# Performance work log

Hardware: AMD Instinct MI355X
Metric: run time of the kernel (lower is better)

## Reference

```python
import jax, jax.numpy as jnp
import numpy as np

EPS = 1e-8       # module eps
LN_EPS = 1e-5    # torch LayerNorm default
TEMP = 1.0       # relevance_temperature
STRENGTH = 1.0   # reweight_strength default (None -> 1.0)

Q, W, A = 64, 16, 64
D, C, H = 512, 512, 512


def _ln(x, g, b):
    m = x.mean(-1, keepdims=True)
    v = ((x - m) ** 2).mean(-1, keepdims=True)
    return (x - m) / jnp.sqrt(v + LN_EPS) * g + b


def _mlp(x, g, b, w1, b1, w2, b2):
    # LayerNorm -> Linear -> GELU(exact) -> Linear
    h = jax.nn.gelu(_ln(x, g, b) @ w1 + b1, approximate=False)
    return h @ w2 + b2


def setup_inputs() -> dict:
    key = jax.random.key(0)
    ks = iter(jax.random.split(key, 40))
    s = 0.02

    def lin(din, dout):
        return (jax.random.normal(next(ks), (din, dout), jnp.float32) * s,
                jnp.zeros((dout,), jnp.float32))

    inp = {
        "query_atoms": jax.random.normal(next(ks), (Q, A, D), jnp.float32),
        "query_masses": jax.random.uniform(next(ks), (Q, A), jnp.float32, 0.01, 1.0),
        "class_atoms": jax.random.normal(next(ks), (W, A, D), jnp.float32),
        "class_masses": jax.random.uniform(next(ks), (W, A), jnp.float32, 0.01, 1.0),
        "class_summary": jax.random.normal(next(ks), (W, C), jnp.float32),
        "episode_context": jax.random.normal(next(ks), (W, C), jnp.float32),
    }
    # query_proj
    inp["qg"], inp["qb"] = jnp.ones((D,), jnp.float32), jnp.zeros((D,), jnp.float32)
    inp["qw1"], inp["qb1"] = lin(D, H)
    inp["qw2"], inp["qb2"] = lin(H, H)
    # atom_proj
    inp["ag"], inp["ab"] = jnp.ones((D,), jnp.float32), jnp.zeros((D,), jnp.float32)
    inp["aw1"], inp["ab1"] = lin(D, H)
    inp["aw2"], inp["ab2"] = lin(H, H)
    # context_proj (input 2*C)
    inp["cg"], inp["cb"] = jnp.ones((2 * C,), jnp.float32), jnp.zeros((2 * C,), jnp.float32)
    inp["cw1"], inp["cb1"] = lin(2 * C, H)
    inp["cw2"], inp["cb2"] = lin(H, H)
    # relevance_head (input 4*H, output 1)
    inp["rg"], inp["rb"] = jnp.ones((4 * H,), jnp.float32), jnp.zeros((4 * H,), jnp.float32)
    inp["rw1"], inp["rb1"] = lin(4 * H, H)
    inp["rw2"], inp["rb2"] = lin(H, 1)
    return inp


def reference(query_atoms, query_masses, class_atoms, class_masses,
              class_summary, episode_context,
              qg, qb, qw1, qb1, qw2, qb2,
              ag, ab, aw1, ab1, aw2, ab2,
              cg, cb, cw1, cb1, cw2, cb2,
              rg, rb, rw1, rb1, rw2, rb2):
    # normalize query masses, pool query atoms -> [Q, D]
    qm = jnp.maximum(query_masses, 0.0)
    qm = qm / jnp.maximum(qm.sum(-1, keepdims=True), EPS)
    pooled = jnp.einsum('qa,qad->qd', qm, query_atoms)

    qh = _mlp(pooled, qg, qb, qw1, qb1, qw2, qb2)            # [Q, H]
    ah = _mlp(class_atoms, ag, ab, aw1, ab1, aw2, ab2)       # [W, A, H]
    ch = _mlp(jnp.concatenate([class_summary, episode_context], -1),
              cg, cb, cw1, cb1, cw2, cb2)                    # [W, H]

    nq, (way, na, h) = qh.shape[0], ah.shape
    a4 = jnp.broadcast_to(ah[None], (nq, way, na, h))
    q4 = jnp.broadcast_to(qh[:, None, None, :], (nq, way, na, h))
    c4 = jnp.broadcast_to(ch[None, :, None, :], (nq, way, na, h))
    fused = jnp.concatenate([a4, q4, a4 * q4, jnp.abs(a4 - q4) + c4], -1)  # [Q,W,A,4H]

    relevance = _mlp(fused, rg, rb, rw1, rb1, rw2, rb2)[..., 0]  # [Q, W, A]

    combined = jnp.log(jnp.maximum(class_masses, EPS))[None] + relevance / TEMP
    rew = jax.nn.softmax(combined, axis=-1)
    mixed = (1.0 - STRENGTH) * class_masses[None] + STRENGTH * rew
    mixed = mixed / jnp.maximum(mixed.sum(-1, keepdims=True), EPS)
    entropy = -(mixed * jnp.log(jnp.maximum(mixed, EPS))).sum(-1)  # [Q, W]
    return mixed, entropy
```

## Files before the change

kernel.cpp:

```cpp
#include <hip/hip_runtime.h>


#define DEV static __device__ __forceinline__

typedef __attribute__((ext_vector_type(8))) __bf16 bf16x8;
typedef __attribute__((ext_vector_type(4))) float f32x4;
typedef unsigned short ushort_t;

DEV ushort_t f2bf(float f) {
  unsigned u = __builtin_bit_cast(unsigned, f);
  u = (u + 0x7fffu + ((u >> 16) & 1u)) >> 16;
  return (ushort_t)u;
}

DEV float gelu_fast(float x) {
  const float y = x * 0.70710678118654752f;
  const float z = fabsf(y);
  const float t = __fdividef(1.0f, 1.0f + 0.3275911f * z);
  float p = 1.061405429f;
  p = p * t - 1.453152027f;
  p = p * t + 1.421413741f;
  p = p * t - 0.284496736f;
  p = p * t + 0.254829592f;
  const float e = 1.0f - p * t * __expf(-z * z);
  const float erfv = copysignf(e, y);
  return 0.5f * x * (1.0f + erfv);
}

DEV float gelu_sig(float x) {
  return x * __frcp_rn(1.0f + __expf(-1.702f * x));
}

#define OFF_XQB    0
#define OFF_XAB    16384
#define OFF_XCB    278528
#define OFF_HAB    286720
#define OFF_HQB    548864
#define OFF_HCB    565248
#define OFF_AHB    569344
#define OFF_QH     1093632
#define OFF_S1     1126400
#define OFF_B1     1126912
#define OFF_WT2    1127424
#define OFF_RW1LOT 1389568
#define OFF_RW1MIT 1520640
#define OFF_AW1T   1651712
#define OFF_QW1T   1782784
#define OFF_CW1T   1913856
#define OFF_AW2T   2176000
#define OFF_QW2T   2307072
#define OFF_CW2T   2438144
#define OFF_YA     OFF_AW1T
#define OFF_YQ     OFF_AW2T
#define OFF_CHH    OFF_XCB
#define OFF_AHHS   OFF_XAB
#define OFF_QHS    OFF_XQB


DEV void transpose_tile(const float* __restrict__ src, int koff, int kt, int ct,
                        ushort_t* __restrict__ dst, int ldk, float* sh, int tid) {
  float (*t)[65] = (float(*)[65])sh;
  for (int idx = tid; idx < 4096; idx += 512) {
    const int r = idx >> 6, c = idx & 63;
    t[r][c] = src[(koff + kt + r) * 512 + ct + c];
  }
  __syncthreads();
  for (int idx = tid; idx < 4096; idx += 512) {
    const int c = idx >> 6, r = idx & 63;
    dst[(ct + c) * ldk + kt + r] = f2bf(t[r][c]);
  }
}

__global__ __launch_bounds__(512) void pre0_kernel(
    const float* __restrict__ qa, const float* __restrict__ qm,
    const float* __restrict__ ca, const float* __restrict__ csum,
    const float* __restrict__ ectx,
    const float* __restrict__ qg, const float* __restrict__ qb,
    const float* __restrict__ ag, const float* __restrict__ ab,
    const float* __restrict__ cg, const float* __restrict__ cb,
    const float* __restrict__ rw1, const float* __restrict__ rg,
    const float* __restrict__ rb,
    const float* __restrict__ aw1, const float* __restrict__ qw1,
    const float* __restrict__ cw1, const float* __restrict__ aw2,
    const float* __restrict__ qw2, const float* __restrict__ cw2,
    float* __restrict__ ws) {
  __shared__ float sh[4160];
  const int b = blockIdx.x, tid = threadIdx.x, l = tid & 63, wv = tid >> 6;

  if (b < 128) {
    ushort_t* WT = (ushort_t*)(ws + OFF_WT2);
    float (*t)[65] = (float(*)[65])sh;
    const int kt = (b >> 3) << 6;
    const int ct = (b & 7) << 6;
    for (int idx = tid; idx < 4096; idx += 512) {
      const int r = idx >> 6, c = idx & 63;
      t[r][c] = rg[1024 + kt + r] * rw1[(1024 + kt + r) * 512 + ct + c];
    }
    __syncthreads();
    for (int idx = tid; idx < 4096; idx += 512) {
      const int c = idx >> 6, r = idx & 63;
      const int n = ct + c, k2 = kt + r;
      WT[((k2 >> 5) << 14) + (n << 5) + (k2 & 31)] = f2bf(t[r][c]);
    }
  } else if (b < 192) {
    const int bb = b - 128;
    transpose_tile(rw1, 0, (bb >> 3) << 6, (bb & 7) << 6,
                   (ushort_t*)(ws + OFF_RW1LOT), 512, sh, tid);
  } else if (b < 256) {
    const int bb = b - 192;
    transpose_tile(rw1, 512, (bb >> 3) << 6, (bb & 7) << 6,
                   (ushort_t*)(ws + OFF_RW1MIT), 512, sh, tid);
  } else if (b < 320) {
    const int bb = b - 256;
    transpose_tile(aw1, 0, (bb >> 3) << 6, (bb & 7) << 6,
                   (ushort_t*)(ws + OFF_AW1T), 512, sh, tid);
  } else if (b < 384) {
    const int bb = b - 320;
    transpose_tile(qw1, 0, (bb >> 3) << 6, (bb & 7) << 6,
                   (ushort_t*)(ws + OFF_QW1T), 512, sh, tid);
  } else if (b < 512) {
    const int bb = b - 384;
    transpose_tile(cw1, 0, (bb >> 3) << 6, (bb & 7) << 6,
                   (ushort_t*)(ws + OFF_CW1T), 1024, sh, tid);
  } else if (b < 576) {
    const int bb = b - 512;
    transpose_tile(aw2, 0, (bb >> 3) << 6, (bb & 7) << 6,
                   (ushort_t*)(ws + OFF_AW2T), 512, sh, tid);
  } else if (b < 640) {
    const int bb = b - 576;
    transpose_tile(qw2, 0, (bb >> 3) << 6, (bb & 7) << 6,
                   (ushort_t*)(ws + OFF_QW2T), 512, sh, tid);
  } else if (b < 704) {
    const int bb = b - 640;
    transpose_tile(cw2, 0, (bb >> 3) << 6, (bb & 7) << 6,
                   (ushort_t*)(ws + OFF_CW2T), 512, sh, tid);
  } else if (b < 720) {
    const int kc = (b - 704) << 7;
    float s0 = 0.f, s1 = 0.f, b0 = 0.f, b1v = 0.f;
    for (int k = kc; k < kc + 128; k += 2) {
      const float wa = rw1[(k << 9) + tid];
      const float wb = rw1[((k + 1) << 9) + tid];
      s0 += rg[k] * wa; b0 += rb[k] * wa;
      s1 += rg[k + 1] * wb; b1v += rb[k + 1] * wb;
    }
    atomicAdd(ws + OFF_S1 + tid, s0 + s1);
    atomicAdd(ws + OFF_B1 + tid, b0 + b1v);
  } else if (b < 784) {
    const int q = b - 720;
    if (wv == 0) {
      float m = fmaxf(qm[(q << 6) + l], 0.f);
      sh[l] = m;
      float s = m;
#pragma unroll
      for (int off = 1; off < 64; off <<= 1) s += __shfl_xor(s, off);
      if (l == 0) sh[64] = 1.0f / fmaxf(s, 1e-8f);
    }
    __syncthreads();
    const float sinv = sh[64];
    const float* qaq = qa + (q << 15) + tid;
    float v0 = 0.f, v1 = 0.f, v2 = 0.f, v3 = 0.f;
#pragma unroll 4
    for (int a = 0; a < 64; a += 4) {
      v0 += sh[a] * qaq[a << 9];
      v1 += sh[a + 1] * qaq[(a + 1) << 9];
      v2 += sh[a + 2] * qaq[(a + 2) << 9];
      v3 += sh[a + 3] * qaq[(a + 3) << 9];
    }
    const float v = (v0 + v1 + v2 + v3) * sinv;
    float s = v, ss = v * v;
#pragma unroll
    for (int off = 1; off < 64; off <<= 1) {
      s += __shfl_xor(s, off); ss += __shfl_xor(ss, off);
    }
    if (l == 0) { sh[128 + wv] = s; sh[136 + wv] = ss; }
    __syncthreads();
    float st = 0.f, sst = 0.f;
#pragma unroll
    for (int i = 0; i < 8; ++i) { st += sh[128 + i]; sst += sh[136 + i]; }
    const float mu = st * (1.0f / 512.0f);
    const float rstd = rsqrtf(sst * (1.0f / 512.0f) - mu * mu + 1e-5f);
    ((ushort_t*)(ws + OFF_XQB))[(q << 9) + tid] =
        f2bf((v - mu) * rstd * qg[tid] + qb[tid]);
  } else if (b < 912) {
    const int row = ((b - 784) << 3) + wv;
    const float* crow = ca + (row << 9);
    float x[8];
    float s = 0.f, ss = 0.f;
#pragma unroll
    for (int i = 0; i < 8; ++i) {
      x[i] = crow[l + (i << 6)];
      s += x[i]; ss += x[i] * x[i];
    }
#pragma unroll
    for (int off = 1; off < 64; off <<= 1) {
      s += __shfl_xor(s, off); ss += __shfl_xor(ss, off);
    }
    const float mu = s * (1.0f / 512.0f);
    const float rstd = rsqrtf(ss * (1.0f / 512.0f) - mu * mu + 1e-5f);
    ushort_t* xab = (ushort_t*)(ws + OFF_XAB);
#pragma unroll
    for (int i = 0; i < 8; ++i) {
      const int k = l + (i << 6);
      xab[(row << 9) + k] = f2bf((x[i] - mu) * rstd * ag[k] + ab[k]);
    }
  } else {
    const int w = b - 912;
    const float v0 = csum[(w << 9) + tid];
    const float v1 = ectx[(w << 9) + tid];
    float s = v0 + v1, ss = v0 * v0 + v1 * v1;
#pragma unroll
    for (int off = 1; off < 64; off <<= 1) {
      s += __shfl_xor(s, off); ss += __shfl_xor(ss, off);
    }
    if (l == 0) { sh[wv] = s; sh[8 + wv] = ss; }
    __syncthreads();
    float st = 0.f, sst = 0.f;
#pragma unroll
    for (int i = 0; i < 8; ++i) { st += sh[i]; sst += sh[8 + i]; }
    const float mu = st * (1.0f / 1024.0f);
    const float rstd = rsqrtf(sst * (1.0f / 1024.0f) - mu * mu + 1e-5f);
    ushort_t* xcb = (ushort_t*)(ws + OFF_XCB);
    xcb[(w << 10) + tid] = f2bf((v0 - mu) * rstd * cg[tid] + cb[tid]);
    xcb[(w << 10) + 512 + tid] =
        f2bf((v1 - mu) * rstd * cg[512 + tid] + cb[512 + tid]);
  }
}

template <int PHASE>
__global__ __launch_bounds__(256) void gemm_kernel(
    float* __restrict__ ws, const float* __restrict__ ba,
    const float* __restrict__ bq, const float* __restrict__ bc,
    const float* __restrict__ rg) {
  const int b = blockIdx.x, tid = threadIdx.x;
  const int l = tid & 63, wv = tid >> 6;

  const ushort_t* A; const ushort_t* BT;
  float* outF = nullptr; ushort_t* outB = nullptr; ushort_t* outS = nullptr;
  ushort_t* outU = nullptr;
  const float* bias = nullptr; const float* scl = nullptr;
  int M, K, t;

  if (PHASE == 1) {
    if (b < 128) {
      A = (const ushort_t*)(ws + OFF_XAB); BT = (const ushort_t*)(ws + OFF_AW1T);
      M = 1024; K = 512; outB = (ushort_t*)(ws + OFF_HAB); bias = ba;
      t = (b << 2) + wv;
    } else if (b < 136) {
      A = (const ushort_t*)(ws + OFF_XQB); BT = (const ushort_t*)(ws + OFF_QW1T);
      M = 64; K = 512; outB = (ushort_t*)(ws + OFF_HQB); bias = bq;
      t = ((b - 128) << 2) + wv;
    } else {
      A = (const ushort_t*)(ws + OFF_XCB); BT = (const ushort_t*)(ws + OFF_CW1T);
      M = 16; K = 1024; outB = (ushort_t*)(ws + OFF_HCB); bias = bc;
      t = ((b - 136) << 2) + wv;
    }
  } else if (PHASE == 2) {
    if (b < 128) {
      A = (const ushort_t*)(ws + OFF_HAB); BT = (const ushort_t*)(ws + OFF_AW2T);
      M = 1024; K = 512; outU = (ushort_t*)(ws + OFF_AHB);
      outS = (ushort_t*)(ws + OFF_AHHS); bias = ba; scl = rg;
      t = (b << 2) + wv;
    } else if (b < 136) {
      A = (const ushort_t*)(ws + OFF_HQB); BT = (const ushort_t*)(ws + OFF_QW2T);
      M = 64; K = 512; outF = ws + OFF_QH;
      outS = (ushort_t*)(ws + OFF_QHS); bias = bq; scl = rg + 512;
      t = ((b - 128) << 2) + wv;
    } else {
      A = (const ushort_t*)(ws + OFF_HCB); BT = (const ushort_t*)(ws + OFF_CW2T);
      M = 16; K = 512; outF = ws + OFF_CHH; bias = bc;
      t = ((b - 136) << 2) + wv;
    }
  } else {
    if (b < 128) {
      A = (const ushort_t*)(ws + OFF_AHHS); BT = (const ushort_t*)(ws + OFF_RW1LOT);
      M = 1024; K = 512; outF = ws + OFF_YA;
      t = (b << 2) + wv;
    } else {
      A = (const ushort_t*)(ws + OFF_QHS); BT = (const ushort_t*)(ws + OFF_RW1MIT);
      M = 64; K = 512; outF = ws + OFF_YQ;
      t = ((b - 128) << 2) + wv;
    }
  }

  const int rt = t >> 4, ct = t & 15;
  const int r0 = rt << 5, c0 = ct << 5;
  const int kh = (l >> 4) << 3;
  const ushort_t* ap[2];
  const ushort_t* bp[2];
#pragma unroll
  for (int fr = 0; fr < 2; ++fr) {
    int r = r0 + (fr << 4) + (l & 15);
    if (r > M - 1) r = M - 1;
    ap[fr] = A + r * K + kh;
  }
#pragma unroll
  for (int cf = 0; cf < 2; ++cf)
    bp[cf] = BT + (c0 + (cf << 4) + (l & 15)) * K + kh;

  f32x4 acc[2][2] = {};
  const int nst = K >> 5;
#pragma unroll 4
  for (int ks = 0; ks < nst; ++ks) {
    bf16x8 afr[2], bfr[2];
#pragma unroll
    for (int fr = 0; fr < 2; ++fr)
      afr[fr] = __builtin_bit_cast(bf16x8, *(const uint4*)(ap[fr] + (ks << 5)));
#pragma unroll
    for (int cf = 0; cf < 2; ++cf)
      bfr[cf] = __builtin_bit_cast(bf16x8, *(const uint4*)(bp[cf] + (ks << 5)));
#pragma unroll
    for (int fr = 0; fr < 2; ++fr)
#pragma unroll
      for (int cf = 0; cf < 2; ++cf)
        acc[fr][cf] = __builtin_amdgcn_mfma_f32_16x16x32_bf16(
            afr[fr], bfr[cf], acc[fr][cf], 0, 0, 0);
  }

  const int rsub = (l >> 4) << 2, cl = l & 15;
#pragma unroll
  for (int fr = 0; fr < 2; ++fr) {
#pragma unroll
    for (int cf = 0; cf < 2; ++cf) {
      const int col = c0 + (cf << 4) + cl;
#pragma unroll
      for (int j = 0; j < 4; ++j) {
        const int row = r0 + (fr << 4) + rsub + j;
        if (row < M) {
          float v = acc[fr][cf][j];
          if (PHASE == 1) {
            outB[(row << 9) + col] = f2bf(gelu_fast(v + bias[col]));
          } else if (PHASE == 2) {
            v += bias[col];
            if (outU) outU[(row << 9) + col] = f2bf(v);
            if (outF) outF[(row << 9) + col] = v;
            if (outS) outS[(row << 9) + col] = f2bf(v * scl[col]);
          } else {
            outF[(row << 9) + col] = v;
          }
        }
      }
    }
  }
}

__global__ __launch_bounds__(512, 2) void main_kernel(
    const ushort_t* __restrict__ AHB, const float* __restrict__ QH,
    const float* __restrict__ CH, const ushort_t* __restrict__ WT2,
    const float* __restrict__ Ya, const float* __restrict__ Yq,
    const float* __restrict__ S1, const float* __restrict__ B1,
    const float* __restrict__ rb1, const float* __restrict__ rw2,
    const float* __restrict__ rb2, const float* __restrict__ cmass,
    float* __restrict__ out) {
  extern __shared__ char smem_raw[];
  float* qs = (float*)smem_raw;
  float* cs = qs + 1024;
  float* s1_s = cs + 512;
  float* s2_s = s1_s + 128;
  float* rel_s = s2_s + 128;
  float* misc = rel_s + 128;
  uint4* ab4 = (uint4*)(smem_raw + 8192);
  uint4* apv = (uint4*)(smem_raw + 8192 + 65536);

  const int tid = threadIdx.x;
  const int l = tid & 63;
  const int wv = tid >> 6;
  const int w = blockIdx.x & 15;
  const int q0 = (blockIdx.x >> 4) << 1;

  {
    const uint4* src = (const uint4*)(AHB + ((w << 6) << 9));
#pragma unroll
    for (int i = 0; i < 16; ++i) {
      const int u = tid + (i << 9);
      const int row = u >> 7, c16 = u & 127;
      ab4[(row << 7) + (c16 ^ (row & 7))] = src[u];
    }
  }
  qs[tid] = QH[(q0 << 9) + tid];
  qs[tid + 512] = QH[(q0 << 9) + 512 + tid];
  cs[tid] = CH[(w << 9) + tid];
  if (tid < 128) { s1_s[tid] = 0.f; s2_s[tid] = 0.f; rel_s[tid] = 0.f; }
  __syncthreads();

  const int p = wv >> 2;
  const int s = wv & 3;
  const int rloc = (s << 4) + (l & 15);
  const float* qsrc = qs + (p << 9);
  const int kh = (l >> 4) << 3;
  const int ar_base = rloc << 7;
  const int rsw = rloc & 7;
  float s1a = 0.f, s2a = 0.f;

#define BUILD(C, B) do { \
    _Pragma("unroll") for (int ksl_ = 0; ksl_ < 4; ++ksl_) { \
      const int kg_ = ((C) << 7) + (ksl_ << 5) + kh; \
      const int ka_ = kg_ & 511; \
      const bf16x8 av8_ = __builtin_bit_cast(bf16x8, \
          ab4[ar_base + ((ka_ >> 3) ^ rsw)]); \
      union { __bf16 bv[8]; uint4 u4; } pk_; \
      _Pragma("unroll") for (int h_ = 0; h_ < 2; ++h_) { \
        const float4 qv_ = *(const float4*)(qsrc + ka_ + (h_ << 2)); \
        const float a0_ = (float)av8_[(h_ << 2) + 0]; \
        const float a1_ = (float)av8_[(h_ << 2) + 1]; \
        const float a2_ = (float)av8_[(h_ << 2) + 2]; \
        const float a3_ = (float)av8_[(h_ << 2) + 3]; \
        float v0_, v1_, v2_, v3_; \
        if ((C) < 4) { \
          v0_ = a0_ * qv_.x; v1_ = a1_ * qv_.y; \
          v2_ = a2_ * qv_.z; v3_ = a3_ * qv_.w; \
          s1a += (a0_ + a1_ + a2_ + a3_) + (v0_ + v1_ + v2_ + v3_); \
          s2a += (a0_ * a0_ + a1_ * a1_ + a2_ * a2_ + a3_ * a3_) + \
                 (v0_ * v0_ + v1_ * v1_ + v2_ * v2_ + v3_ * v3_); \
        } else { \
          const float4 c_ = *(const float4*)(cs + ka_ + (h_ << 2)); \
          v0_ = fabsf(a0_ - qv_.x) + c_.x; \
          v1_ = fabsf(a1_ - qv_.y) + c_.y; \
          v2_ = fabsf(a2_ - qv_.z) + c_.z; \
          v3_ = fabsf(a3_ - qv_.w) + c_.w; \
          s1a += v0_ + v1_ + v2_ + v3_; \
          s2a += v0_ * v0_ + v1_ * v1_ + v2_ * v2_ + v3_ * v3_; \
        } \
        pk_.bv[(h_ << 2) + 0] = (__bf16)v0_; \
        pk_.bv[(h_ << 2) + 1] = (__bf16)v1_; \
        pk_.bv[(h_ << 2) + 2] = (__bf16)v2_; \
        pk_.bv[(h_ << 2) + 3] = (__bf16)v3_; \
      } \
      apv[((B) << 11) + (p << 10) + (ksl_ << 8) + (s << 6) + l] = pk_.u4; \
    } } while (0)

  BUILD(0, 0);
  if ((wv & 3) == 0) {
    float sq = 0.f, sqq = 0.f;
#pragma unroll
    for (int it = 0; it < 8; ++it) {
      const float vq = qsrc[l + (it << 6)];
      sq += vq; sqq += vq * vq;
    }
#pragma unroll
    for (int off = 1; off < 64; off <<= 1) {
      sq += __shfl_xor(sq, off); sqq += __shfl_xor(sqq, off);
    }
    if (l == 0) { misc[(p << 1)] = sq; misc[(p << 1) + 1] = sqq; }
  }
  __syncthreads();

  f32x4 acc0[4][4] = {}, acc1[4][4] = {};
  const int ncb = (wv << 6) + (l & 15);
  const int boff = (ncb << 5) + kh;
#pragma unroll
  for (int c = 0; c < 8; ++c) {
    if (c < 7) {
      BUILD(c + 1, (c + 1) & 1);
    } else {
      s1a += __shfl_xor(s1a, 16); s1a += __shfl_xor(s1a, 32);
      s2a += __shfl_xor(s2a, 16); s2a += __shfl_xor(s2a, 32);
      if ((l >> 4) == 0) {
        atomicAdd(&s1_s[(p << 6) + rloc], s1a);
        atomicAdd(&s2_s[(p << 6) + rloc], s2a);
      }
    }
    const uint4* cbuf = apv + ((c & 1) << 11);
    const ushort_t* wb = WT2 + ((c << 2) << 14) + boff;
    uint4 bn0 = *(const uint4*)(wb);
    uint4 bn1 = *(const uint4*)(wb + (16 << 5));
    uint4 bn2 = *(const uint4*)(wb + (32 << 5));
    uint4 bn3 = *(const uint4*)(wb + (48 << 5));
#pragma unroll
    for (int ksl = 0; ksl < 4; ++ksl) {
      const bf16x8 bf0 = __builtin_bit_cast(bf16x8, bn0);
      const bf16x8 bf1 = __builtin_bit_cast(bf16x8, bn1);
      const bf16x8 bf2 = __builtin_bit_cast(bf16x8, bn2);
      const bf16x8 bf3 = __builtin_bit_cast(bf16x8, bn3);
      if (ksl < 3) {
        const ushort_t* wn = wb + ((ksl + 1) << 14);
        bn0 = *(const uint4*)(wn);
        bn1 = *(const uint4*)(wn + (16 << 5));
        bn2 = *(const uint4*)(wn + (32 << 5));
        bn3 = *(const uint4*)(wn + (48 << 5));
      }
      bf16x8 afr;
      __builtin_amdgcn_s_setprio(1);
#pragma unroll
      for (int fr = 0; fr < 4; ++fr) {
        afr = __builtin_bit_cast(bf16x8, cbuf[(ksl << 8) + (fr << 6) + l]);
        acc0[fr][0] = __builtin_amdgcn_mfma_f32_16x16x32_bf16(afr, bf0, acc0[fr][0], 0, 0, 0);
        acc0[fr][1] = __builtin_amdgcn_mfma_f32_16x16x32_bf16(afr, bf1, acc0[fr][1], 0, 0, 0);
        acc0[fr][2] = __builtin_amdgcn_mfma_f32_16x16x32_bf16(afr, bf2, acc0[fr][2], 0, 0, 0);
        acc0[fr][3] = __builtin_amdgcn_mfma_f32_16x16x32_bf16(afr, bf3, acc0[fr][3], 0, 0, 0);
      }
#pragma unroll
      for (int fr = 0; fr < 4; ++fr) {
        afr = __builtin_bit_cast(bf16x8, cbuf[(1 << 10) + (ksl << 8) + (fr << 6) + l]);
        acc1[fr][0] = __builtin_amdgcn_mfma_f32_16x16x32_bf16(afr, bf0, acc1[fr][0], 0, 0, 0);
        acc1[fr][1] = __builtin_amdgcn_mfma_f32_16x16x32_bf16(afr, bf1, acc1[fr][1], 0, 0, 0);
        acc1[fr][2] = __builtin_amdgcn_mfma_f32_16x16x32_bf16(afr, bf2, acc1[fr][2], 0, 0, 0);
        acc1[fr][3] = __builtin_amdgcn_mfma_f32_16x16x32_bf16(afr, bf3, acc1[fr][3], 0, 0, 0);
      }
      __builtin_amdgcn_s_setprio(0);
    }
    __syncthreads();
  }
#undef BUILD

  if (tid < 128) {
    const int pp = tid >> 6;
    const float s1r = s1_s[tid] + misc[pp << 1];
    const float s2r = s2_s[tid] + misc[(pp << 1) + 1];
    const float mu = s1r * (1.0f / 2048.0f);
    const float rs = rsqrtf(s2r * (1.0f / 2048.0f) - mu * mu + 1e-5f);
    s1_s[tid] = mu;
    s2_s[tid] = rs;
  }
  __syncthreads();

  {
    float yqv0[4], yqv1[4], s1c[4], b1c[4], w2c[4];
#pragma unroll
    for (int cf = 0; cf < 4; ++cf) {
      const int n = ncb + (cf << 4);
      yqv0[cf] = Yq[(q0 << 9) + n];
      yqv1[cf] = Yq[((q0 + 1) << 9) + n];
      s1c[cf] = S1[n];
      b1c[cf] = B1[n] + rb1[n];
      w2c[cf] = rw2[n];
    }
    const float* yab = Ya + (w << 15) + ncb;
    const int rsub = (l >> 4) << 2;
#pragma unroll
    for (int fr = 0; fr < 4; ++fr) {
#pragma unroll
      for (int j = 0; j < 4; ++j) {
        const int r = (fr << 4) + rsub + j;
        const float mu0 = s1_s[r], rs0 = s2_s[r];
        const float mu1 = s1_s[64 + r], rs1 = s2_s[64 + r];
        float rp0 = 0.f, rp1 = 0.f;
#pragma unroll
        for (int cf = 0; cf < 4; ++cf) {
          const float ya = yab[(r << 9) + (cf << 4)];
          const float c0v = ya + yqv0[cf] - mu0 * s1c[cf];
          const float c1v = ya + yqv1[cf] - mu1 * s1c[cf];
          rp0 += gelu_sig(fmaf(rs0, acc0[fr][cf][j] + c0v, b1c[cf])) * w2c[cf];
          rp1 += gelu_sig(fmaf(rs1, acc1[fr][cf][j] + c1v, b1c[cf])) * w2c[cf];
        }
        rp0 += __shfl_xor(rp0, 1); rp0 += __shfl_xor(rp0, 2);
        rp0 += __shfl_xor(rp0, 4); rp0 += __shfl_xor(rp0, 8);
        rp1 += __shfl_xor(rp1, 1); rp1 += __shfl_xor(rp1, 2);
        rp1 += __shfl_xor(rp1, 4); rp1 += __shfl_xor(rp1, 8);
        if ((l & 15) == 0) {
          atomicAdd(&rel_s[r], rp0);
          atomicAdd(&rel_s[64 + r], rp1);
        }
      }
    }
  }
  __syncthreads();

  if (tid < 128) {
    const int pp = tid >> 6, a = tid & 63;
    const int qw = ((q0 + pp) << 4) + w;
    const float relv = rel_s[(pp << 6) + a] + rb2[0];
    const float x = logf(fmaxf(cmass[(w << 6) + a], 1e-8f)) + relv;
    float m = x;
#pragma unroll
    for (int off = 1; off < 64; off <<= 1) m = fmaxf(m, __shfl_xor(m, off));
    const float pv = expf(x - m);
    float sv = pv;
#pragma unroll
    for (int off = 1; off < 64; off <<= 1) sv += __shfl_xor(sv, off);
    float mix = pv / fmaxf(sv, 1e-8f);
    float s2 = mix;
#pragma unroll
    for (int off = 1; off < 64; off <<= 1) s2 += __shfl_xor(s2, off);
    mix = mix / fmaxf(s2, 1e-8f);
    const float et = -mix * logf(fmaxf(mix, 1e-8f));
    float ent = et;
#pragma unroll
    for (int off = 1; off < 64; off <<= 1) ent += __shfl_xor(ent, off);
    out[(qw << 6) + a] = mix;
    if (a == 0) out[65536 + qw] = ent;
  }
}

extern "C" void kernel_launch(void* const* d_in, const int* in_sizes, int n_in,
                              void* d_out, int out_size, void* d_ws, size_t ws_size,
                              hipStream_t stream) {
  (void)in_sizes; (void)n_in; (void)out_size; (void)ws_size;
  const float* q_atoms = (const float*)d_in[0];
  const float* q_mass  = (const float*)d_in[1];
  const float* c_atoms = (const float*)d_in[2];
  const float* c_mass  = (const float*)d_in[3];
  const float* c_sum   = (const float*)d_in[4];
  const float* e_ctx   = (const float*)d_in[5];
  const float* qg  = (const float*)d_in[6];  const float* qb  = (const float*)d_in[7];
  const float* qw1 = (const float*)d_in[8];  const float* qb1 = (const float*)d_in[9];
  const float* qw2 = (const float*)d_in[10]; const float* qb2 = (const float*)d_in[11];
  const float* ag  = (const float*)d_in[12]; const float* ab  = (const float*)d_in[13];
  const float* aw1 = (const float*)d_in[14]; const float* ab1 = (const float*)d_in[15];
  const float* aw2 = (const float*)d_in[16]; const float* ab2 = (const float*)d_in[17];
  const float* cg  = (const float*)d_in[18]; const float* cb  = (const float*)d_in[19];
  const float* cw1 = (const float*)d_in[20]; const float* cb1 = (const float*)d_in[21];
  const float* cw2 = (const float*)d_in[22]; const float* cb2 = (const float*)d_in[23];
  const float* rg  = (const float*)d_in[24]; const float* rb  = (const float*)d_in[25];
  const float* rw1 = (const float*)d_in[26]; const float* rb1 = (const float*)d_in[27];
  const float* rw2 = (const float*)d_in[28]; const float* rb2 = (const float*)d_in[29];

  float* ws = (float*)d_ws;
  float* out = (float*)d_out;

  hipMemsetAsync(ws + OFF_S1, 0, 1024 * sizeof(float), stream);
  pre0_kernel<<<928, 512, 0, stream>>>(q_atoms, q_mass, c_atoms, c_sum, e_ctx,
                                       qg, qb, ag, ab, cg, cb, rw1, rg, rb,
                                       aw1, qw1, cw1, aw2, qw2, cw2, ws);
  gemm_kernel<1><<<140, 256, 0, stream>>>(ws, ab1, qb1, cb1, rg);
  gemm_kernel<2><<<140, 256, 0, stream>>>(ws, ab2, qb2, cb2, rg);
  gemm_kernel<3><<<136, 256, 0, stream>>>(ws, nullptr, nullptr, nullptr, rg);

  static const size_t MAIN_SMEM = 8192 + 65536 + 65536;
  hipFuncSetAttribute((const void*)main_kernel,
                      hipFuncAttributeMaxDynamicSharedMemorySize, (int)MAIN_SMEM);
  main_kernel<<<512, 512, MAIN_SMEM, stream>>>(
      (const ushort_t*)(ws + OFF_AHB), ws + OFF_QH, ws + OFF_CHH,
      (const ushort_t*)(ws + OFF_WT2), ws + OFF_YA, ws + OFF_YQ,
      ws + OFF_S1, ws + OFF_B1, rb1, rw2, rb2, c_mass, out);
}
```

Before: 149.3 us.

## Fold second MLP weights into relevance head to remove a GEMM launch

Precomputes combined weight products (rg-scaled rw1 blocks times aw2/qw2) in phase 1, so Ya/Yq are computed directly from the hidden activations in phase 2 alongside the other second-layer GEMMs. This removes the separate third GEMM kernel launch and its serial dependency, and adds bias-folding terms via atomics in pre0. The cost is extra weight-product GEMM work each call, plus additional bf16 rounding of the fused weight product, which may shift numerics.

```diff
diff --git a/kernel.cpp b/kernel.cpp
--- a/kernel.cpp
+++ b/kernel.cpp
@@ -38,6 +38,8 @@
 #define OFF_HQB    548864
 #define OFF_HCB    565248
 #define OFF_AHB    569344
+#define OFF_WAYAT  831488
+#define OFF_WQYQT  962560
 #define OFF_QH     1093632
 #define OFF_S1     1126400
 #define OFF_B1     1126912
@@ -50,19 +52,23 @@
 #define OFF_AW2T   2176000
 #define OFF_QW2T   2307072
 #define OFF_CW2T   2438144
+#define OFF_YQ2    2569216
+#define OFF_AW2B   2601984
+#define OFF_QW2B   2733056
+#define OFF_BYA    2864128
+#define OFF_BYQ    2864640
 #define OFF_YA     OFF_AW1T
-#define OFF_YQ     OFF_AW2T
 #define OFF_CHH    OFF_XCB
-#define OFF_AHHS   OFF_XAB
-#define OFF_QHS    OFF_XQB
 
 
 DEV void transpose_tile(const float* __restrict__ src, int koff, int kt, int ct,
-                        ushort_t* __restrict__ dst, int ldk, float* sh, int tid) {
+                        ushort_t* __restrict__ dst, int ldk, float* sh, int tid,
+                        const float* __restrict__ scl) {
   float (*t)[65] = (float(*)[65])sh;
   for (int idx = tid; idx < 4096; idx += 512) {
     const int r = idx >> 6, c = idx & 63;
-    t[r][c] = src[(koff + kt + r) * 512 + ct + c];
+    const float s = scl ? scl[koff + kt + r] : 1.0f;
+    t[r][c] = s * src[(koff + kt + r) * 512 + ct + c];
   }
   __syncthreads();
   for (int idx = tid; idx < 4096; idx += 512) {
@@ -83,6 +89,7 @@
     const float* __restrict__ aw1, const float* __restrict__ qw1,
     const float* __restrict__ cw1, const float* __restrict__ aw2,
     const float* __restrict__ qw2, const float* __restrict__ cw2,
+    const float* __restrict__ ab2, const float* __restrict__ qb2,
     float* __restrict__ ws) {
   __shared__ float sh[4160];
   const int b = blockIdx.x, tid = threadIdx.x, l = tid & 63, wv = tid >> 6;
@@ -105,46 +112,49 @@
   } else if (b < 192) {
     const int bb = b - 128;
     transpose_tile(rw1, 0, (bb >> 3) << 6, (bb & 7) << 6,
-                   (ushort_t*)(ws + OFF_RW1LOT), 512, sh, tid);
+                   (ushort_t*)(ws + OFF_RW1LOT), 512, sh, tid, rg);
   } else if (b < 256) {
     const int bb = b - 192;
     transpose_tile(rw1, 512, (bb >> 3) << 6, (bb & 7) << 6,
-                   (ushort_t*)(ws + OFF_RW1MIT), 512, sh, tid);
+                   (ushort_t*)(ws + OFF_RW1MIT), 512, sh, tid, rg);
   } else if (b < 320) {
     const int bb = b - 256;
     transpose_tile(aw1, 0, (bb >> 3) << 6, (bb & 7) << 6,
-                   (ushort_t*)(ws + OFF_AW1T), 512, sh, tid);
+                   (ushort_t*)(ws + OFF_AW1T), 512, sh, tid, nullptr);
   } else if (b < 384) {
     const int bb = b - 320;
     transpose_tile(qw1, 0, (bb >> 3) << 6, (bb & 7) << 6,
-                   (ushort_t*)(ws + OFF_QW1T), 512, sh, tid);
+                   (ushort_t*)(ws + OFF_QW1T), 512, sh, tid, nullptr);
   } else if (b < 512) {
     const int bb = b - 384;
     transpose_tile(cw1, 0, (bb >> 3) << 6, (bb & 7) << 6,
-                   (ushort_t*)(ws + OFF_CW1T), 1024, sh, tid);
+                   (ushort_t*)(ws + OFF_CW1T), 1024, sh, tid, nullptr);
   } else if (b < 576) {
     const int bb = b - 512;
     transpose_tile(aw2, 0, (bb >> 3) << 6, (bb & 7) << 6,
-                   (ushort_t*)(ws + OFF_AW2T), 512, sh, tid);
+                   (ushort_t*)(ws + OFF_AW2T), 512, sh, tid, nullptr);
   } else if (b < 640) {
     const int bb = b - 576;
     transpose_tile(qw2, 0, (bb >> 3) << 6, (bb & 7) << 6,
-                   (ushort_t*)(ws + OFF_QW2T), 512, sh, tid);
+                   (ushort_t*)(ws + OFF_QW2T), 512, sh, tid, nullptr);
   } else if (b < 704) {
     const int bb = b - 640;
     transpose_tile(cw2, 0, (bb >> 3) << 6, (bb & 7) << 6,
-                   (ushort_t*)(ws + OFF_CW2T), 512, sh, tid);
+                   (ushort_t*)(ws + OFF_CW2T), 512, sh, tid, nullptr);
   } else if (b < 720) {
     const int kc = (b - 704) << 7;
-    float s0 = 0.f, s1 = 0.f, b0 = 0.f, b1v = 0.f;
-    for (int k = kc; k < kc + 128; k += 2) {
-      const float wa = rw1[(k << 9) + tid];
-      const float wb = rw1[((k + 1) << 9) + tid];
-      s0 += rg[k] * wa; b0 += rb[k] * wa;
-      s1 += rg[k + 1] * wb; b1v += rb[k + 1] * wb;
-    }
-    atomicAdd(ws + OFF_S1 + tid, s0 + s1);
-    atomicAdd(ws + OFF_B1 + tid, b0 + b1v);
+    float s0 = 0.f, b0 = 0.f, y0 = 0.f;
+    for (int k = kc; k < kc + 128; ++k) {
+      const float wval = rw1[(k << 9) + tid];
+      s0 += rg[k] * wval;
+      b0 += rb[k] * wval;
+      if (b < 708)       y0 += ab2[k] * rg[k] * wval;
+      else if (b < 712)  y0 += qb2[k - 512] * rg[k] * wval;
+    }
+    atomicAdd(ws + OFF_S1 + tid, s0);
+    atomicAdd(ws + OFF_B1 + tid, b0);
+    if (b < 708)      atomicAdd(ws + OFF_BYA + tid, y0);
+    else if (b < 712) atomicAdd(ws + OFF_BYQ + tid, y0);
   } else if (b < 784) {
     const int q = b - 720;
     if (wv == 0) {
@@ -203,7 +213,7 @@
       const int k = l + (i << 6);
       xab[(row << 9) + k] = f2bf((x[i] - mu) * rstd * ag[k] + ab[k]);
     }
-  } else {
+  } else if (b < 928) {
     const int w = b - 912;
     const float v0 = csum[(w << 9) + tid];
     const float v1 = ectx[(w << 9) + tid];
@@ -223,21 +233,39 @@
     xcb[(w << 10) + tid] = f2bf((v0 - mu) * rstd * cg[tid] + cb[tid]);
     xcb[(w << 10) + 512 + tid] =
         f2bf((v1 - mu) * rstd * cg[512 + tid] + cb[512 + tid]);
+  } else if (b < 992) {
+    const int base = ((b - 928) << 12) + (tid << 3);
+    const float4 v0 = *(const float4*)(aw2 + base);
+    const float4 v1 = *(const float4*)(aw2 + base + 4);
+    union { __bf16 bv[8]; uint4 u4; } pk;
+    pk.bv[0] = (__bf16)v0.x; pk.bv[1] = (__bf16)v0.y;
+    pk.bv[2] = (__bf16)v0.z; pk.bv[3] = (__bf16)v0.w;
+    pk.bv[4] = (__bf16)v1.x; pk.bv[5] = (__bf16)v1.y;
+    pk.bv[6] = (__bf16)v1.z; pk.bv[7] = (__bf16)v1.w;
+    *(uint4*)((ushort_t*)(ws + OFF_AW2B) + base) = pk.u4;
+  } else {
+    const int base = ((b - 992) << 12) + (tid << 3);
+    const float4 v0 = *(const float4*)(qw2 + base);
+    const float4 v1 = *(const float4*)(qw2 + base + 4);
+    union { __bf16 bv[8]; uint4 u4; } pk;
+    pk.bv[0] = (__bf16)v0.x; pk.bv[1] = (__bf16)v0.y;
+    pk.bv[2] = (__bf16)v0.z; pk.bv[3] = (__bf16)v0.w;
+    pk.bv[4] = (__bf16)v1.x; pk.bv[5] = (__bf16)v1.y;
+    pk.bv[6] = (__bf16)v1.z; pk.bv[7] = (__bf16)v1.w;
+    *(uint4*)((ushort_t*)(ws + OFF_QW2B) + base) = pk.u4;
   }
 }
 
 template <int PHASE>
 __global__ __launch_bounds__(256) void gemm_kernel(
     float* __restrict__ ws, const float* __restrict__ ba,
-    const float* __restrict__ bq, const float* __restrict__ bc,
-    const float* __restrict__ rg) {
+    const float* __restrict__ bq, const float* __restrict__ bc) {
   const int b = blockIdx.x, tid = threadIdx.x;
   const int l = tid & 63, wv = tid >> 6;
 
   const ushort_t* A; const ushort_t* BT;
-  float* outF = nullptr; ushort_t* outB = nullptr; ushort_t* outS = nullptr;
-  ushort_t* outU = nullptr;
-  const float* bias = nullptr; const float* scl = nullptr;
+  float* outF = nullptr; ushort_t* outB = nullptr; ushort_t* outU = nullptr;
+  const float* bias = nullptr;
   int M, K, t;
 
   if (PHASE == 1) {
@@ -249,36 +277,40 @@
       A = (const ushort_t*)(ws + OFF_XQB); BT = (const ushort_t*)(ws + OFF_QW1T);
       M = 64; K = 512; outB = (ushort_t*)(ws + OFF_HQB); bias = bq;
       t = ((b - 128) << 2) + wv;
-    } else {
+    } else if (b < 140) {
       A = (const ushort_t*)(ws + OFF_XCB); BT = (const ushort_t*)(ws + OFF_CW1T);
       M = 16; K = 1024; outB = (ushort_t*)(ws + OFF_HCB); bias = bc;
       t = ((b - 136) << 2) + wv;
-    }
-  } else if (PHASE == 2) {
+    } else if (b < 204) {
+      A = (const ushort_t*)(ws + OFF_RW1LOT); BT = (const ushort_t*)(ws + OFF_AW2B);
+      M = 512; K = 512; outB = (ushort_t*)(ws + OFF_WAYAT); bias = nullptr;
+      t = ((b - 140) << 2) + wv;
+    } else {
+      A = (const ushort_t*)(ws + OFF_RW1MIT); BT = (const ushort_t*)(ws + OFF_QW2B);
+      M = 512; K = 512; outB = (ushort_t*)(ws + OFF_WQYQT); bias = nullptr;
+      t = ((b - 204) << 2) + wv;
+    }
+  } else {
     if (b < 128) {
       A = (const ushort_t*)(ws + OFF_HAB); BT = (const ushort_t*)(ws + OFF_AW2T);
-      M = 1024; K = 512; outU = (ushort_t*)(ws + OFF_AHB);
-      outS = (ushort_t*)(ws + OFF_AHHS); bias = ba; scl = rg;
+      M = 1024; K = 512; outU = (ushort_t*)(ws + OFF_AHB); bias = ba;
       t = (b << 2) + wv;
     } else if (b < 136) {
       A = (const ushort_t*)(ws + OFF_HQB); BT = (const ushort_t*)(ws + OFF_QW2T);
-      M = 64; K = 512; outF = ws + OFF_QH;
-      outS = (ushort_t*)(ws + OFF_QHS); bias = bq; scl = rg + 512;
+      M = 64; K = 512; outF = ws + OFF_QH; bias = bq;
       t = ((b - 128) << 2) + wv;
-    } else {
+    } else if (b < 140) {
       A = (const ushort_t*)(ws + OFF_HCB); BT = (const ushort_t*)(ws + OFF_CW2T);
       M = 16; K = 512; outF = ws + OFF_CHH; bias = bc;
       t = ((b - 136) << 2) + wv;
-    }
-  } else {
-    if (b < 128) {
-      A = (const ushort_t*)(ws + OFF_AHHS); BT = (const ushort_t*)(ws + OFF_RW1LOT);
-      M = 1024; K = 512; outF = ws + OFF_YA;
-      t = (b << 2) + wv;
+    } else if (b < 268) {
+      A = (const ushort_t*)(ws + OFF_HAB); BT = (const ushort_t*)(ws + OFF_WAYAT);
+      M = 1024; K = 512; outF = ws + OFF_YA; bias = ws + OFF_BYA;
+      t = ((b - 140) << 2) + wv;
     } else {
-      A = (const ushort_t*)(ws + OFF_QHS); BT = (const ushort_t*)(ws + OFF_RW1MIT);
-      M = 64; K = 512; outF = ws + OFF_YQ;
-      t = ((b - 128) << 2) + wv;
+      A = (const ushort_t*)(ws + OFF_HQB); BT = (const ushort_t*)(ws + OFF_WQYQT);
+      M = 64; K = 512; outF = ws + OFF_YQ2; bias = ws + OFF_BYQ;
+      t = ((b - 268) << 2) + wv;
     }
   }
 
@@ -328,14 +360,12 @@
         if (row < M) {
           float v = acc[fr][cf][j];
           if (PHASE == 1) {
-            outB[(row << 9) + col] = f2bf(gelu_fast(v + bias[col]));
-          } else if (PHASE == 2) {
+            outB[(row << 9) + col] =
+                bias ? f2bf(gelu_fast(v + bias[col])) : f2bf(v);
+          } else {
             v += bias[col];
             if (outU) outU[(row << 9) + col] = f2bf(v);
-            if (outF) outF[(row << 9) + col] = v;
-            if (outS) outS[(row << 9) + col] = f2bf(v * scl[col]);
-          } else {
-            outF[(row << 9) + col] = v;
+            else      outF[(row << 9) + col] = v;
           }
         }
       }
@@ -608,18 +638,19 @@
   float* out = (float*)d_out;
 
   hipMemsetAsync(ws + OFF_S1, 0, 1024 * sizeof(float), stream);
-  pre0_kernel<<<928, 512, 0, stream>>>(q_atoms, q_mass, c_atoms, c_sum, e_ctx,
-                                       qg, qb, ag, ab, cg, cb, rw1, rg, rb,
-                                       aw1, qw1, cw1, aw2, qw2, cw2, ws);
-  gemm_kernel<1><<<140, 256, 0, stream>>>(ws, ab1, qb1, cb1, rg);
-  gemm_kernel<2><<<140, 256, 0, stream>>>(ws, ab2, qb2, cb2, rg);
-  gemm_kernel<3><<<136, 256, 0, stream>>>(ws, nullptr, nullptr, nullptr, rg);
+  hipMemsetAsync(ws + OFF_BYA, 0, 1024 * sizeof(float), stream);
+  pre0_kernel<<<1056, 512, 0, stream>>>(q_atoms, q_mass, c_atoms, c_sum, e_ctx,
+                                        qg, qb, ag, ab, cg, cb, rw1, rg, rb,
+                                        aw1, qw1, cw1, aw2, qw2, cw2,
+                                        ab2, qb2, ws);
+  gemm_kernel<1><<<268, 256, 0, stream>>>(ws, ab1, qb1, cb1);
+  gemm_kernel<2><<<276, 256, 0, stream>>>(ws, ab2, qb2, cb2);
 
   static const size_t MAIN_SMEM = 8192 + 65536 + 65536;
   hipFuncSetAttribute((const void*)main_kernel,
                       hipFuncAttributeMaxDynamicSharedMemorySize, (int)MAIN_SMEM);
   main_kernel<<<512, 512, MAIN_SMEM, stream>>>(
       (const ushort_t*)(ws + OFF_AHB), ws + OFF_QH, ws + OFF_CHH,
-      (const ushort_t*)(ws + OFF_WT2), ws + OFF_YA, ws + OFF_YQ,
+      (const ushort_t*)(ws + OFF_WT2), ws + OFF_YA, ws + OFF_YQ2,
       ws + OFF_S1, ws + OFF_B1, rb1, rw2, rb2, c_mass, out);
 }
```

Result: slower. 177.9 us (+19.2%).
